# Kernel tuning notes

Hardware: AMD Instinct MI355X
Metric: run time of the kernel (lower is better)

Reference implementation:

```python
import jax, jax.numpy as jnp
import numpy as np

SR = 16000
FLEN = 400        # round(winlen * samplerate)
STEP = 160        # round(winstep * samplerate)
NFFT = 512
NFILT = 26
NUMCEP = 13
PREEMPH = 0.97
CEPLIFTER = 22
LOWFREQ = 0.0
HIGHFREQ = SR / 2.0
EPS = float(np.finfo(np.float32).eps)


def _hz2mel(hz):
    return 2595.0 * np.log10(1.0 + hz / 700.0)


def _mel2hz(mel):
    return 700.0 * (10.0 ** (mel / 2595.0) - 1.0)


def _filterbanks():
    # [NFFT//2+1, NFILT] mel triangular filterbank (transposed, as used in torch.mm)
    melpoints = np.linspace(_hz2mel(LOWFREQ), _hz2mel(HIGHFREQ), NFILT + 2)
    bins = np.floor((NFFT + 1) * _mel2hz(melpoints) / SR)
    fb = np.zeros([NFILT, NFFT // 2 + 1], dtype=np.float64)
    for j in range(NFILT):
        for i in range(int(bins[j]), int(bins[j + 1])):
            fb[j, i] = (i - bins[j]) / (bins[j + 1] - bins[j])
        for i in range(int(bins[j + 1]), int(bins[j + 2])):
            fb[j, i] = (bins[j + 2] - i) / (bins[j + 2] - bins[j + 1])
    return fb.T  # [257, 26]


def _dct_mat(N, k):
    # orthonormal DCT-II matrix rows 0..k-1: [k, N]
    n = np.arange(N)
    kk = np.arange(k)[:, None]
    C = np.cos(np.pi * (2 * n[None, :] + 1) * kk / (2.0 * N))
    C[0] *= 1.0 / np.sqrt(N)
    C[1:] *= np.sqrt(2.0 / N)
    return C


def setup_inputs() -> dict:
    key = jax.random.key(0)
    k1, k2 = jax.random.split(key)
    signals = jax.random.normal(k1, (64, 320000), dtype=jnp.float32)
    lengths = jax.random.randint(k2, (64,), 0, 320000, dtype=jnp.int32)
    return {"signals": signals, "lengths": lengths}


def reference(signals, lengths):
    B, T = signals.shape
    F = 1 if T <= FLEN else 1 + int(np.ceil((T - FLEN) / float(STEP)))
    padlen = (F - 1) * STEP + FLEN

    # preemphasis (uses self.preemph=0.97), masked past each sample's length
    pre = jnp.concatenate(
        [signals[:, :1], signals[:, 1:] - PREEMPH * signals[:, :-1]], axis=1)
    pos = jnp.arange(T)
    pre = jnp.where(pos[None, :] < lengths[:, None], pre, jnp.zeros((), pre.dtype))

    # framing: [B, F, FLEN]
    pad = jnp.pad(pre, ((0, 0), (0, padlen - T)))
    idx = np.arange(FLEN)[None, :] + STEP * np.arange(F)[:, None]
    frames = pad[:, idx]

    # power spectrum, [B, F, NFFT//2+1]
    spec = jnp.fft.rfft(frames, n=NFFT, axis=-1)
    pspec = (spec.real * spec.real + spec.imag * spec.imag) / NFFT
    energy = pspec.sum(-1) + EPS                      # [B, F]

    fb = jnp.asarray(_filterbanks(), dtype=signals.dtype)     # [257, 26]
    feat = jnp.log(pspec @ fb + EPS)                  # [B, F, 26]

    dctm = jnp.asarray(_dct_mat(NFILT, NUMCEP), dtype=signals.dtype)  # [13, 26]
    ceps = jnp.einsum('bfn,kn->bfk', feat, dctm)      # [B, F, 13]

    n = jnp.arange(NUMCEP, dtype=signals.dtype)
    lift = 1.0 + (CEPLIFTER / 2.0) * jnp.sin(np.pi * n / CEPLIFTER)
    ceps = ceps * lift
    ceps = ceps.at[:, :, 0].set(jnp.log(energy))       # appendEnergy

    # per-sample number of frames; zero-pad rest (original pads to batch max)
    nframes = jnp.where(
        lengths <= FLEN, 1,
        1 + jnp.ceil((lengths - FLEN) / float(STEP)).astype(jnp.int32))
    fmask = jnp.arange(F)[None, :] < nframes[:, None]
    ceps = jnp.where(fmask[:, :, None], ceps, jnp.zeros((), ceps.dtype))
    return ceps, nframes
```

## Files before the change

kernel.cpp:

```cpp
#include <hip/hip_runtime.h>
#include <math.h>

#define SRATE   16000
#define FLEN    400
#define STEP    160
#define NFFT    512
#define NBINS   257
#define NFILT   26
#define NUMCEP  13
#define BATCH   64
#define TLEN    320000
#define NFRAMES 1999
#define NPAIRS  1000
#define EPSF    1.1920929e-07f
#define PI_F    3.14159265358979323846f

typedef float    v2f __attribute__((ext_vector_type(2)));
typedef unsigned uv2 __attribute__((ext_vector_type(2)));

__device__ __forceinline__ v2f mk2(float a, float b) { v2f v; v.x = a; v.y = b; return v; }
__device__ __forceinline__ v2f pfma(v2f a, v2f b, v2f c) { return __builtin_elementwise_fma(a, b, c); }

template<int CTRL>
__device__ __forceinline__ float fdpp(float x) {
    return __builtin_bit_cast(float, __builtin_amdgcn_mov_dpp(
        __builtin_bit_cast(int, x), CTRL, 0xF, 0xF, true));
}
template<int IMM>
__device__ __forceinline__ float fswz(float x) {
    return __builtin_bit_cast(float, __builtin_amdgcn_ds_swizzle(
        __builtin_bit_cast(int, x), IMM));
}
__device__ __forceinline__ uv2 pl32(float x) {
    unsigned u = __builtin_bit_cast(unsigned, x);
    return __builtin_amdgcn_permlane32_swap(u, u, false, false);
}
__device__ __forceinline__ float fxor32(float x, bool hi32) {
    uv2 r = pl32(x);
    return __builtin_bit_cast(float, hi32 ? r[0] : r[1]);
}
#define DPP_X1   0xB1
#define DPP_X2   0x4E
#define DPP_X8   0x128
#define SWZ_X4   0x101F
#define SWZ_X16  0x401F

__global__ void mfcc_setup_kernel(const int* __restrict__ lengths,
                                  void* __restrict__ ws,
                                  float* __restrict__ out_nframes) {
    int tid = threadIdx.x;
    int*   bins = (int*)ws;
    float* dctw = (float*)ws + 32;

    if (tid < 28) {
        double M    = 2595.0 * log10(1.0 + 8000.0 / 700.0);
        double step = M / 27.0;
        double mel  = (tid == 27) ? M : (double)tid * step;
        double hz   = 700.0 * (pow(10.0, mel / 2595.0) - 1.0);
        bins[tid] = (int)floor((double)(NFFT + 1) * hz / (double)SRATE);
    }
    for (int t = tid; t < NUMCEP * NFILT; t += 64) {
        int k = t / NFILT, j = t - k * NFILT;
        double v = cos(M_PI * (double)((2 * j + 1) * k) / (2.0 * (double)NFILT));
        v *= (k == 0) ? 1.0 / sqrt((double)NFILT) : sqrt(2.0 / (double)NFILT);
        double lift = 1.0 + 11.0 * sin(M_PI * (double)k / 22.0);
        dctw[t] = (float)(v * lift);
    }
    if (tid < BATCH) {
        int len = lengths[tid];
        int nf  = (len <= FLEN) ? 1 : 1 + (len - FLEN + STEP - 1) / STEP;
        out_nframes[tid] = (float)nf;
    }
}

__launch_bounds__(256)
__global__ void mfcc_kernel(const float* __restrict__ sig,
                            const int*   __restrict__ lengths,
                            const void*  __restrict__ ws,
                            float*       __restrict__ out) {
    __shared__ float ps0[4][NBINS + 3];
    __shared__ float ps1[4][NBINS + 3];
    __shared__ float feat0[4][28], feat1[4][28];
    __shared__ float dctS[NUMCEP * NFILT];
    __shared__ int   binsS[NFILT + 2];

    const int tid  = threadIdx.x;
    const int lane = tid & 63;
    const int w    = tid >> 6;

    {
        const int*   binsG = (const int*)ws;
        const float* dctG  = (const float*)ws + 32;
        for (int t = tid; t < NUMCEP * NFILT; t += 256) dctS[t] = dctG[t];
        if (tid < NFILT + 2) binsS[tid] = binsG[tid];
    }
    __syncthreads();

    const int gp = blockIdx.x * 4 + w;
    const int b  = gp / NPAIRS;
    const int g  = gp - b * NPAIRS;
    const int f0 = 2 * g;
    const int f1 = f0 + 1;
    const int len = lengths[b];
    const int nf  = (len <= FLEN) ? 1 : 1 + (len - FLEN + STEP - 1) / STEP;

    if (f0 >= nf) {
        int k = lane & 31;
        bool hi = lane >= 32;
        int f = hi ? f1 : f0;
        if (k < NUMCEP && f < NFRAMES)
            out[((long)b * NFRAMES + f) * NUMCEP + k] = 0.0f;
        return;
    }

    const float* s = sig + (long)b * TLEN;
    const int base = f0 * STEP;

    const int B   = (int)(__brev((unsigned)lane) >> 26);
    const int i0  = 8 * B;
    const bool liveB = (i0 < FLEN);

    v2f Zr[4], Zi[4];
    const bool fastw = (base >= 1) && (base + 560 <= len);
    if (fastw) {
        float w0[9], w1[9];
        if (liveB) {
            const int tb0 = base + i0 - 1;
            #pragma unroll
            for (int j = 0; j < 9; ++j) {
                w0[j] = s[tb0 + j];
                w1[j] = s[tb0 + STEP + j];
            }
        } else {
            #pragma unroll
            for (int j = 0; j < 9; ++j) { w0[j] = 0.0f; w1[j] = 0.0f; }
        }
        #pragma unroll
        for (int m = 0; m < 4; ++m) {
            const int j = (m == 0) ? 0 : (m == 1) ? 4 : (m == 2) ? 2 : 6;
            Zr[m] = mk2(fmaf(-0.97f, w0[j],     w0[j + 1]),
                        fmaf(-0.97f, w0[j + 1], w0[j + 2]));
            Zi[m] = mk2(fmaf(-0.97f, w1[j],     w1[j + 1]),
                        fmaf(-0.97f, w1[j + 1], w1[j + 2]));
        }
    } else {
        float w0[9], w1[9];
        const int tb0 = base + i0 - 1;
        const int tb1 = tb0 + STEP;
        #pragma unroll
        for (int j = 0; j < 9; ++j) {
            int t0 = tb0 + j;
            w0[j] = (liveB && t0 >= 0 && t0 < len) ? s[t0] : 0.0f;
            int t1 = tb1 + j;
            w1[j] = (liveB && t1 < len) ? s[t1] : 0.0f;
        }
        const int tbe = base + i0;
        #pragma unroll
        for (int m = 0; m < 4; ++m) {
            const int j = (m == 0) ? 0 : (m == 1) ? 4 : (m == 2) ? 2 : 6;
            float v0a = fmaf(-0.97f, w0[j],     w0[j + 1]);
            float v0b = fmaf(-0.97f, w0[j + 1], w0[j + 2]);
            float v1a = fmaf(-0.97f, w1[j],     w1[j + 1]);
            float v1b = fmaf(-0.97f, w1[j + 1], w1[j + 2]);
            bool ma = liveB && (tbe + j) < len;
            bool mb = liveB && (tbe + j + 1) < len;
            bool na = liveB && (tbe + STEP + j) < len;
            bool nb = liveB && (tbe + STEP + j + 1) < len;
            Zr[m] = mk2(ma ? v0a : 0.0f, mb ? v0b : 0.0f);
            Zi[m] = mk2(na ? v1a : 0.0f, nb ? v1b : 0.0f);
        }
    }

    const float ang = -PI_F * (float)lane / 256.0f;
    float T1i = __sinf(ang);
    float T1r = __cosf(ang);
#define SQC(orr, oii, ir, ii) { float _r = ir * ir - ii * ii; oii = 2.0f * ir * ii; orr = _r; }
    float T2r, T2i;   SQC(T2r, T2i, T1r, T1i)
    float T4r, T4i;   SQC(T4r, T4i, T2r, T2i)
    float T8r, T8i;   SQC(T8r, T8i, T4r, T4i)
    float T16r, T16i; SQC(T16r, T16i, T8r, T8i)
    float T32r, T32i; SQC(T32r, T32i, T16r, T16i)
    float T64r, T64i; SQC(T64r, T64i, T32r, T32i)
    float T128r, T128i; SQC(T128r, T128i, T64r, T64i)
    const float RH = 0.70710678118654752f;
    const float A1r = RH * (T1r + T1i), A1i = RH * (T1i - T1r);
    const float A2r = T1i,              A2i = -T1r;
    const float A3r = RH * (T1i - T1r), A3i = -RH * (T1r + T1i);

    {
        const float sg = (lane & 1) ? -1.0f : 1.0f;
        const v2f sg2 = mk2(sg, sg);
        #pragma unroll
        for (int m = 0; m < 4; ++m) {
            v2f pr = mk2(fdpp<DPP_X1>(Zr[m].x), fdpp<DPP_X1>(Zr[m].y));
            v2f pi = mk2(fdpp<DPP_X1>(Zi[m].x), fdpp<DPP_X1>(Zi[m].y));
            Zr[m] = pfma(sg2, Zr[m], pr);
            Zi[m] = pfma(sg2, Zi[m], pi);
        }
    }

#define PK_XSTAGE_G(d, UR, UI, SH)                                            \
    {                                                                         \
        const bool hi_ = (lane & (d)) != 0;                                   \
        const float ur = hi_ ? (UR) : 1.0f;                                   \
        const float ui = hi_ ? (UI) : 0.0f;                                   \
        const float sg = hi_ ? 1.0f : -1.0f;                                  \
        const v2f ur2 = mk2(ur, ur), ui2 = mk2(ui, ui);                       \
        const v2f nui2 = mk2(-ui, -ui), sg2 = mk2(sg, sg);                    \
        _Pragma("unroll")                                                     \
        for (int m = 0; m < 4; ++m) {                                         \
            v2f tr = pfma(Zi[m], nui2, Zr[m] * ur2);                          \
            v2f ti = pfma(Zi[m], ur2,  Zr[m] * ui2);                          \
            v2f pr = mk2(SH(tr.x), SH(tr.y));                                 \
            v2f pi = mk2(SH(ti.x), SH(ti.y));                                 \
            Zr[m] = pfma(sg2, pr, tr);                                        \
            Zi[m] = pfma(sg2, pi, ti);                                        \
        }                                                                     \
    }
#define SH_X2(v)  fdpp<DPP_X2>(v)
#define SH_X4(v)  fswz<SWZ_X4>(v)
#define SH_X8(v)  fdpp<DPP_X8>(v)
#define SH_X16(v) fswz<SWZ_X16>(v)
#define SH_X32(v) fxor32(v, hi_)
    PK_XSTAGE_G(2,  T128r, T128i, SH_X2)
    PK_XSTAGE_G(4,  T64r,  T64i,  SH_X4)
    PK_XSTAGE_G(8,  T32r,  T32i,  SH_X8)
    PK_XSTAGE_G(16, T16r,  T16i,  SH_X16)
    PK_XSTAGE_G(32, T8r,   T8i,   SH_X32)

#define PBFLY(A, Bv, WR, WI)                                                  \
    {                                                                         \
        const v2f wr2 = mk2((WR), (WR)), wi2 = mk2((WI), (WI));               \
        const v2f nwi2 = mk2(-(WI), -(WI));                                   \
        v2f tr = pfma(Zi[Bv], nwi2, Zr[Bv] * wr2);                            \
        v2f ti = pfma(Zi[Bv], wr2,  Zr[Bv] * wi2);                            \
        Zr[Bv] = Zr[A] - tr;  Zi[Bv] = Zi[A] - ti;                            \
        Zr[A]  = Zr[A] + tr;  Zi[A]  = Zi[A] + ti;                            \
    }
    PBFLY(0, 1, T4r, T4i)
    PBFLY(2, 3, T4r, T4i)
    PBFLY(0, 2, T2r, T2i)
    PBFLY(1, 3, T2i, -T2r)

    float zr[8], zi[8];
    {
        #pragma unroll
        for (int m = 0; m < 4; ++m) {
            const float Wr = (m == 0) ? T1r : (m == 1) ? A1r : (m == 2) ? A2r : A3r;
            const float Wi = (m == 0) ? T1i : (m == 1) ? A1i : (m == 2) ? A2i : A3i;
            float tr = Zr[m].y * Wr - Zi[m].y * Wi;
            float ti = Zr[m].y * Wi + Zi[m].y * Wr;
            zr[m]     = Zr[m].x + tr;  zi[m]     = Zi[m].x + ti;
            zr[m + 4] = Zr[m].x - tr;  zi[m + 4] = Zi[m].x - ti;
        }
    }

    float* P0 = ps0[w];
    float* P1 = ps1[w];
    const float inv = 1.0f / (4.0f * (float)NFFT);
    float e0 = 0.0f, e1 = 0.0f;
    const int ml = (64 - lane) & 63;
    #pragma unroll
    for (int r = 0; r < 4; ++r) {
        float mr = __shfl(zr[7 - r], ml);
        float mi = __shfl(zi[7 - r], ml);
        if (lane == 0) { mr = zr[(8 - r) & 7]; mi = zi[(8 - r) & 7]; }
        float ar = zr[r] + mr, ai = zi[r] - mi;
        float br = zi[r] + mi, bi = zr[r] - mr;
        float p0 = (ar * ar + ai * ai) * inv;
        float p1 = (br * br + bi * bi) * inv;
        P0[64 * r + lane] = p0;
        P1[64 * r + lane] = p1;
        e0 += p0; e1 += p1;
    }
    if (lane == 0) {
        float p0 = 4.0f * zr[4] * zr[4] * inv;
        float p1 = 4.0f * zi[4] * zi[4] * inv;
        P0[256] = p0; P1[256] = p1;
        e0 += p0; e1 += p1;
    }
    v2f E = mk2(e0, e1);
    E = E + mk2(fdpp<DPP_X1>(E.x),  fdpp<DPP_X1>(E.y));
    E = E + mk2(fdpp<DPP_X2>(E.x),  fdpp<DPP_X2>(E.y));
    E = E + mk2(fswz<SWZ_X4>(E.x),  fswz<SWZ_X4>(E.y));
    E = E + mk2(fdpp<DPP_X8>(E.x),  fdpp<DPP_X8>(E.y));
    E = E + mk2(fswz<SWZ_X16>(E.x), fswz<SWZ_X16>(E.y));
    {
        uv2 rx = pl32(E.x), ry = pl32(E.y);
        E = mk2(__builtin_bit_cast(float, rx[0]) + __builtin_bit_cast(float, rx[1]),
                __builtin_bit_cast(float, ry[0]) + __builtin_bit_cast(float, ry[1]));
    }
    __builtin_amdgcn_wave_barrier();

    const int  j  = lane & 31;
    const bool hi = lane >= 32;
    {
        const float* P = hi ? P1 : P0;
        float fu = 0.0f, fs = 0.0f, fu2 = 0.0f, fs2 = 0.0f;
        if (j <= NFILT) {
            int bA = binsS[j], bB = binsS[j + 1];
            int i = bA;
            for (; i + 1 < bB; i += 2) {
                float p = P[i], q = P[i + 1];
                fs  += p;  fu  = fmaf(p, (float)(i - bA), fu);
                fs2 += q;  fu2 = fmaf(q, (float)(i + 1 - bA), fu2);
            }
            if (i < bB) {
                float p = P[i];
                fs += p;  fu = fmaf(p, (float)(i - bA), fu);
            }
            fs += fs2;  fu += fu2;
            fu *= (bB > bA) ? 1.0f / (float)(bB - bA) : 0.0f;
        }
        float down  = fs - fu;
        float dnext = __shfl(down, lane + 1);
        if (j < NFILT) {
            float fv = logf(fu + dnext + EPSF);
            if (hi) feat1[w][j] = fv; else feat0[w][j] = fv;
        }
    }
    __builtin_amdgcn_wave_barrier();

    if (j < NUMCEP) {
        const float* ft = hi ? feat1[w] : feat0[w];
        float a0 = 0.0f, a1 = 0.0f;
        #pragma unroll
        for (int jj = 0; jj < NFILT; jj += 2) {
            a0 = fmaf(ft[jj],     dctS[j * NFILT + jj],     a0);
            a1 = fmaf(ft[jj + 1], dctS[j * NFILT + jj + 1], a1);
        }
        float val = a0 + a1;
        if (j == 0) val = logf((hi ? E.y : E.x) + EPSF);
        int f = hi ? f1 : f0;
        if (f < NFRAMES) {
            if (f >= nf) val = 0.0f;
            out[((long)b * NFRAMES + f) * NUMCEP + j] = val;
        }
    }
}

extern "C" void kernel_launch(void* const* d_in, const int* in_sizes, int n_in,
                              void* d_out, int out_size, void* d_ws, size_t ws_size,
                              hipStream_t stream) {
    const float* sig     = (const float*)d_in[0];
    const int*   lengths = (const int*)d_in[1];
    float* out = (float*)d_out;

    mfcc_setup_kernel<<<1, 64, 0, stream>>>(lengths, d_ws,
                                            out + (size_t)BATCH * NFRAMES * NUMCEP);

    const int total_pairs = BATCH * NPAIRS;
    mfcc_kernel<<<total_pairs / 4, 256, 0, stream>>>(sig, lengths, d_ws, out);
}
```

Measured before the change: 56.69 us.

## Process four frames per wavefront with two interleaved packed FFTs

Each wavefront now handles four frames (two real-pair FFTs) instead of two. The FFT stages, power spectrum, filterbank and DCT are interleaved across both pairs with packed v2f math, and the grid shrinks by half. The intent is more independent work per wave to hide DPP/shuffle latency and to amortise twiddle setup, shared-table loads and per-wave overhead. The trade-off is higher register pressure, which may reduce occupancy. It also switches the log calls to fast __logf.

```diff
diff --git a/kernel.cpp b/kernel.cpp
--- a/kernel.cpp
+++ b/kernel.cpp
@@ -11,7 +11,7 @@
 #define BATCH   64
 #define TLEN    320000
 #define NFRAMES 1999
-#define NPAIRS  1000
+#define NGRP    500
 #define EPSF    1.1920929e-07f
 #define PI_F    3.14159265358979323846f
 
@@ -78,9 +78,9 @@
                             const int*   __restrict__ lengths,
                             const void*  __restrict__ ws,
                             float*       __restrict__ out) {
-    __shared__ float ps0[4][NBINS + 3];
-    __shared__ float ps1[4][NBINS + 3];
-    __shared__ float feat0[4][28], feat1[4][28];
+    __shared__ v2f psA[4][260];
+    __shared__ v2f psB[4][260];
+    __shared__ v2f featAs[4][28], featBs[4][28];
     __shared__ float dctS[NUMCEP * NFILT];
     __shared__ int   binsS[NFILT + 2];
 
@@ -96,20 +96,21 @@
     }
     __syncthreads();
 
-    const int gp = blockIdx.x * 4 + w;
-    const int b  = gp / NPAIRS;
-    const int g  = gp - b * NPAIRS;
-    const int f0 = 2 * g;
-    const int f1 = f0 + 1;
+    const int G  = blockIdx.x * 4 + w;
+    const int b  = G / NGRP;
+    const int q  = G - b * NGRP;
+    const int f0 = 4 * q;
     const int len = lengths[b];
     const int nf  = (len <= FLEN) ? 1 : 1 + (len - FLEN + STEP - 1) / STEP;
 
     if (f0 >= nf) {
-        int k = lane & 31;
-        bool hi = lane >= 32;
-        int f = hi ? f1 : f0;
-        if (k < NUMCEP && f < NFRAMES)
-            out[((long)b * NFRAMES + f) * NUMCEP + k] = 0.0f;
+        if (lane < 52) {
+            int d13 = lane / 13;
+            int kk  = lane - 13 * d13;
+            int ff  = f0 + d13;
+            if (ff < NFRAMES)
+                out[((long)b * NFRAMES + ff) * NUMCEP + kk] = 0.0f;
+        }
         return;
     }
 
@@ -120,54 +121,61 @@
     const int i0  = 8 * B;
     const bool liveB = (i0 < FLEN);
 
-    v2f Zr[4], Zi[4];
-    const bool fastw = (base >= 1) && (base + 560 <= len);
+    v2f Zr0[4], Zi0[4], Zr1[4], Zi1[4];
+    const bool fastw = (base >= 1) && (base + 880 <= len);
     if (fastw) {
-        float w0[9], w1[9];
+        float w0[9], w1[9], w2[9], w3[9];
         if (liveB) {
             const int tb0 = base + i0 - 1;
             #pragma unroll
             for (int j = 0; j < 9; ++j) {
                 w0[j] = s[tb0 + j];
-                w1[j] = s[tb0 + STEP + j];
+                w1[j] = s[tb0 + 160 + j];
+                w2[j] = s[tb0 + 320 + j];
+                w3[j] = s[tb0 + 480 + j];
             }
         } else {
             #pragma unroll
-            for (int j = 0; j < 9; ++j) { w0[j] = 0.0f; w1[j] = 0.0f; }
+            for (int j = 0; j < 9; ++j) { w0[j] = w1[j] = w2[j] = w3[j] = 0.0f; }
         }
         #pragma unroll
         for (int m = 0; m < 4; ++m) {
             const int j = (m == 0) ? 0 : (m == 1) ? 4 : (m == 2) ? 2 : 6;
-            Zr[m] = mk2(fmaf(-0.97f, w0[j],     w0[j + 1]),
-                        fmaf(-0.97f, w0[j + 1], w0[j + 2]));
-            Zi[m] = mk2(fmaf(-0.97f, w1[j],     w1[j + 1]),
-                        fmaf(-0.97f, w1[j + 1], w1[j + 2]));
+            Zr0[m] = mk2(fmaf(-0.97f, w0[j],     w0[j + 1]),
+                         fmaf(-0.97f, w0[j + 1], w0[j + 2]));
+            Zi0[m] = mk2(fmaf(-0.97f, w1[j],     w1[j + 1]),
+                         fmaf(-0.97f, w1[j + 1], w1[j + 2]));
+            Zr1[m] = mk2(fmaf(-0.97f, w2[j],     w2[j + 1]),
+                         fmaf(-0.97f, w2[j + 1], w2[j + 2]));
+            Zi1[m] = mk2(fmaf(-0.97f, w3[j],     w3[j + 1]),
+                         fmaf(-0.97f, w3[j + 1], w3[j + 2]));
         }
     } else {
-        float w0[9], w1[9];
+        float w0[9], w1[9], w2[9], w3[9];
         const int tb0 = base + i0 - 1;
-        const int tb1 = tb0 + STEP;
         #pragma unroll
         for (int j = 0; j < 9; ++j) {
             int t0 = tb0 + j;
             w0[j] = (liveB && t0 >= 0 && t0 < len) ? s[t0] : 0.0f;
-            int t1 = tb1 + j;
-            w1[j] = (liveB && t1 < len) ? s[t1] : 0.0f;
+            int t1 = t0 + 160; w1[j] = (liveB && t1 < len) ? s[t1] : 0.0f;
+            int t2 = t0 + 320; w2[j] = (liveB && t2 < len) ? s[t2] : 0.0f;
+            int t3 = t0 + 480; w3[j] = (liveB && t3 < len) ? s[t3] : 0.0f;
         }
         const int tbe = base + i0;
         #pragma unroll
         for (int m = 0; m < 4; ++m) {
             const int j = (m == 0) ? 0 : (m == 1) ? 4 : (m == 2) ? 2 : 6;
-            float v0a = fmaf(-0.97f, w0[j],     w0[j + 1]);
-            float v0b = fmaf(-0.97f, w0[j + 1], w0[j + 2]);
-            float v1a = fmaf(-0.97f, w1[j],     w1[j + 1]);
-            float v1b = fmaf(-0.97f, w1[j + 1], w1[j + 2]);
-            bool ma = liveB && (tbe + j) < len;
-            bool mb = liveB && (tbe + j + 1) < len;
-            bool na = liveB && (tbe + STEP + j) < len;
-            bool nb = liveB && (tbe + STEP + j + 1) < len;
-            Zr[m] = mk2(ma ? v0a : 0.0f, mb ? v0b : 0.0f);
-            Zi[m] = mk2(na ? v1a : 0.0f, nb ? v1b : 0.0f);
+#define ASMW(Wk, OFF, DST)                                                    \
+            { float va = fmaf(-0.97f, Wk[j],     Wk[j + 1]);                  \
+              float vb = fmaf(-0.97f, Wk[j + 1], Wk[j + 2]);                  \
+              bool ma = liveB && (tbe + (OFF) + j)     < len;                 \
+              bool mb = liveB && (tbe + (OFF) + j + 1) < len;                 \
+              DST = mk2(ma ? va : 0.0f, mb ? vb : 0.0f); }
+            ASMW(w0, 0,   Zr0[m])
+            ASMW(w1, 160, Zi0[m])
+            ASMW(w2, 320, Zr1[m])
+            ASMW(w3, 480, Zi1[m])
+#undef ASMW
         }
     }
 
@@ -192,14 +200,21 @@
         const v2f sg2 = mk2(sg, sg);
         #pragma unroll
         for (int m = 0; m < 4; ++m) {
-            v2f pr = mk2(fdpp<DPP_X1>(Zr[m].x), fdpp<DPP_X1>(Zr[m].y));
-            v2f pi = mk2(fdpp<DPP_X1>(Zi[m].x), fdpp<DPP_X1>(Zi[m].y));
-            Zr[m] = pfma(sg2, Zr[m], pr);
-            Zi[m] = pfma(sg2, Zi[m], pi);
-        }
-    }
-
-#define PK_XSTAGE_G(d, UR, UI, SH)                                            \
+            v2f pr = mk2(fdpp<DPP_X1>(Zr0[m].x), fdpp<DPP_X1>(Zr0[m].y));
+            v2f pi = mk2(fdpp<DPP_X1>(Zi0[m].x), fdpp<DPP_X1>(Zi0[m].y));
+            Zr0[m] = pfma(sg2, Zr0[m], pr);
+            Zi0[m] = pfma(sg2, Zi0[m], pi);
+        }
+        #pragma unroll
+        for (int m = 0; m < 4; ++m) {
+            v2f pr = mk2(fdpp<DPP_X1>(Zr1[m].x), fdpp<DPP_X1>(Zr1[m].y));
+            v2f pi = mk2(fdpp<DPP_X1>(Zi1[m].x), fdpp<DPP_X1>(Zi1[m].y));
+            Zr1[m] = pfma(sg2, Zr1[m], pr);
+            Zi1[m] = pfma(sg2, Zi1[m], pi);
+        }
+    }
+
+#define PK_XSTAGE2(d, UR, UI, SH)                                             \
     {                                                                         \
         const bool hi_ = (lane & (d)) != 0;                                   \
         const float ur = hi_ ? (UR) : 1.0f;                                   \
@@ -209,12 +224,21 @@
         const v2f nui2 = mk2(-ui, -ui), sg2 = mk2(sg, sg);                    \
         _Pragma("unroll")                                                     \
         for (int m = 0; m < 4; ++m) {                                         \
-            v2f tr = pfma(Zi[m], nui2, Zr[m] * ur2);                          \
-            v2f ti = pfma(Zi[m], ur2,  Zr[m] * ui2);                          \
+            v2f tr = pfma(Zi0[m], nui2, Zr0[m] * ur2);                        \
+            v2f ti = pfma(Zi0[m], ur2,  Zr0[m] * ui2);                        \
             v2f pr = mk2(SH(tr.x), SH(tr.y));                                 \
             v2f pi = mk2(SH(ti.x), SH(ti.y));                                 \
-            Zr[m] = pfma(sg2, pr, tr);                                        \
-            Zi[m] = pfma(sg2, pi, ti);                                        \
+            Zr0[m] = pfma(sg2, pr, tr);                                       \
+            Zi0[m] = pfma(sg2, pi, ti);                                       \
+        }                                                                     \
+        _Pragma("unroll")                                                     \
+        for (int m = 0; m < 4; ++m) {                                         \
+            v2f tr = pfma(Zi1[m], nui2, Zr1[m] * ur2);                        \
+            v2f ti = pfma(Zi1[m], ur2,  Zr1[m] * ui2);                        \
+            v2f pr = mk2(SH(tr.x), SH(tr.y));                                 \
+            v2f pi = mk2(SH(ti.x), SH(ti.y));                                 \
+            Zr1[m] = pfma(sg2, pr, tr);                                       \
+            Zi1[m] = pfma(sg2, pi, ti);                                       \
         }                                                                     \
     }
 #define SH_X2(v)  fdpp<DPP_X2>(v)
@@ -222,120 +246,137 @@
 #define SH_X8(v)  fdpp<DPP_X8>(v)
 #define SH_X16(v) fswz<SWZ_X16>(v)
 #define SH_X32(v) fxor32(v, hi_)
-    PK_XSTAGE_G(2,  T128r, T128i, SH_X2)
-    PK_XSTAGE_G(4,  T64r,  T64i,  SH_X4)
-    PK_XSTAGE_G(8,  T32r,  T32i,  SH_X8)
-    PK_XSTAGE_G(16, T16r,  T16i,  SH_X16)
-    PK_XSTAGE_G(32, T8r,   T8i,   SH_X32)
-
-#define PBFLY(A, Bv, WR, WI)                                                  \
+    PK_XSTAGE2(2,  T128r, T128i, SH_X2)
+    PK_XSTAGE2(4,  T64r,  T64i,  SH_X4)
+    PK_XSTAGE2(8,  T32r,  T32i,  SH_X8)
+    PK_XSTAGE2(16, T16r,  T16i,  SH_X16)
+    PK_XSTAGE2(32, T8r,   T8i,   SH_X32)
+
+#define PBFLY2(A, Bv, WR, WI)                                                 \
     {                                                                         \
         const v2f wr2 = mk2((WR), (WR)), wi2 = mk2((WI), (WI));               \
         const v2f nwi2 = mk2(-(WI), -(WI));                                   \
-        v2f tr = pfma(Zi[Bv], nwi2, Zr[Bv] * wr2);                            \
-        v2f ti = pfma(Zi[Bv], wr2,  Zr[Bv] * wi2);                            \
-        Zr[Bv] = Zr[A] - tr;  Zi[Bv] = Zi[A] - ti;                            \
-        Zr[A]  = Zr[A] + tr;  Zi[A]  = Zi[A] + ti;                            \
-    }
-    PBFLY(0, 1, T4r, T4i)
-    PBFLY(2, 3, T4r, T4i)
-    PBFLY(0, 2, T2r, T2i)
-    PBFLY(1, 3, T2i, -T2r)
-
-    float zr[8], zi[8];
-    {
-        #pragma unroll
-        for (int m = 0; m < 4; ++m) {
-            const float Wr = (m == 0) ? T1r : (m == 1) ? A1r : (m == 2) ? A2r : A3r;
-            const float Wi = (m == 0) ? T1i : (m == 1) ? A1i : (m == 2) ? A2i : A3i;
-            float tr = Zr[m].y * Wr - Zi[m].y * Wi;
-            float ti = Zr[m].y * Wi + Zi[m].y * Wr;
-            zr[m]     = Zr[m].x + tr;  zi[m]     = Zi[m].x + ti;
-            zr[m + 4] = Zr[m].x - tr;  zi[m + 4] = Zi[m].x - ti;
-        }
-    }
-
-    float* P0 = ps0[w];
-    float* P1 = ps1[w];
+        { v2f tr = pfma(Zi0[Bv], nwi2, Zr0[Bv] * wr2);                        \
+          v2f ti = pfma(Zi0[Bv], wr2,  Zr0[Bv] * wi2);                        \
+          Zr0[Bv] = Zr0[A] - tr;  Zi0[Bv] = Zi0[A] - ti;                      \
+          Zr0[A]  = Zr0[A] + tr;  Zi0[A]  = Zi0[A] + ti; }                    \
+        { v2f tr = pfma(Zi1[Bv], nwi2, Zr1[Bv] * wr2);                        \
+          v2f ti = pfma(Zi1[Bv], wr2,  Zr1[Bv] * wi2);                        \
+          Zr1[Bv] = Zr1[A] - tr;  Zi1[Bv] = Zi1[A] - ti;                      \
+          Zr1[A]  = Zr1[A] + tr;  Zi1[A]  = Zi1[A] + ti; }                    \
+    }
+    PBFLY2(0, 1, T4r, T4i)
+    PBFLY2(2, 3, T4r, T4i)
+    PBFLY2(0, 2, T2r, T2i)
+    PBFLY2(1, 3, T2i, -T2r)
+
+    float zrA[8], ziA[8], zrB[8], ziB[8];
+    #pragma unroll
+    for (int m = 0; m < 4; ++m) {
+        const float Wr = (m == 0) ? T1r : (m == 1) ? A1r : (m == 2) ? A2r : A3r;
+        const float Wi = (m == 0) ? T1i : (m == 1) ? A1i : (m == 2) ? A2i : A3i;
+        { float tr = Zr0[m].y * Wr - Zi0[m].y * Wi;
+          float ti = Zr0[m].y * Wi + Zi0[m].y * Wr;
+          zrA[m]     = Zr0[m].x + tr;  ziA[m]     = Zi0[m].x + ti;
+          zrA[m + 4] = Zr0[m].x - tr;  ziA[m + 4] = Zi0[m].x - ti; }
+        { float tr = Zr1[m].y * Wr - Zi1[m].y * Wi;
+          float ti = Zr1[m].y * Wi + Zi1[m].y * Wr;
+          zrB[m]     = Zr1[m].x + tr;  ziB[m]     = Zi1[m].x + ti;
+          zrB[m + 4] = Zr1[m].x - tr;  ziB[m + 4] = Zi1[m].x - ti; }
+    }
+
+    v2f* PA = psA[w];
+    v2f* PB = psB[w];
     const float inv = 1.0f / (4.0f * (float)NFFT);
-    float e0 = 0.0f, e1 = 0.0f;
+    v2f eA = mk2(0.0f, 0.0f), eB = mk2(0.0f, 0.0f);
     const int ml = (64 - lane) & 63;
     #pragma unroll
     for (int r = 0; r < 4; ++r) {
-        float mr = __shfl(zr[7 - r], ml);
-        float mi = __shfl(zi[7 - r], ml);
-        if (lane == 0) { mr = zr[(8 - r) & 7]; mi = zi[(8 - r) & 7]; }
-        float ar = zr[r] + mr, ai = zi[r] - mi;
-        float br = zi[r] + mi, bi = zr[r] - mr;
-        float p0 = (ar * ar + ai * ai) * inv;
-        float p1 = (br * br + bi * bi) * inv;
-        P0[64 * r + lane] = p0;
-        P1[64 * r + lane] = p1;
-        e0 += p0; e1 += p1;
+        float mrA = __shfl(zrA[7 - r], ml), miA = __shfl(ziA[7 - r], ml);
+        float mrB = __shfl(zrB[7 - r], ml), miB = __shfl(ziB[7 - r], ml);
+        if (lane == 0) {
+            mrA = zrA[(8 - r) & 7]; miA = ziA[(8 - r) & 7];
+            mrB = zrB[(8 - r) & 7]; miB = ziB[(8 - r) & 7];
+        }
+        { float ar = zrA[r] + mrA, ai = ziA[r] - miA;
+          float br = ziA[r] + miA, bi = zrA[r] - mrA;
+          v2f p = mk2((ar * ar + ai * ai) * inv, (br * br + bi * bi) * inv);
+          PA[64 * r + lane] = p;  eA += p; }
+        { float ar = zrB[r] + mrB, ai = ziB[r] - miB;
+          float br = ziB[r] + miB, bi = zrB[r] - mrB;
+          v2f p = mk2((ar * ar + ai * ai) * inv, (br * br + bi * bi) * inv);
+          PB[64 * r + lane] = p;  eB += p; }
     }
     if (lane == 0) {
-        float p0 = 4.0f * zr[4] * zr[4] * inv;
-        float p1 = 4.0f * zi[4] * zi[4] * inv;
-        P0[256] = p0; P1[256] = p1;
-        e0 += p0; e1 += p1;
-    }
-    v2f E = mk2(e0, e1);
-    E = E + mk2(fdpp<DPP_X1>(E.x),  fdpp<DPP_X1>(E.y));
-    E = E + mk2(fdpp<DPP_X2>(E.x),  fdpp<DPP_X2>(E.y));
-    E = E + mk2(fswz<SWZ_X4>(E.x),  fswz<SWZ_X4>(E.y));
-    E = E + mk2(fdpp<DPP_X8>(E.x),  fdpp<DPP_X8>(E.y));
-    E = E + mk2(fswz<SWZ_X16>(E.x), fswz<SWZ_X16>(E.y));
-    {
-        uv2 rx = pl32(E.x), ry = pl32(E.y);
-        E = mk2(__builtin_bit_cast(float, rx[0]) + __builtin_bit_cast(float, rx[1]),
-                __builtin_bit_cast(float, ry[0]) + __builtin_bit_cast(float, ry[1]));
-    }
+        v2f pA = mk2(4.0f * zrA[4] * zrA[4] * inv, 4.0f * ziA[4] * ziA[4] * inv);
+        v2f pB = mk2(4.0f * zrB[4] * zrB[4] * inv, 4.0f * ziB[4] * ziB[4] * inv);
+        PA[256] = pA;  eA += pA;
+        PB[256] = pB;  eB += pB;
+    }
+#define ERED(E)                                                               \
+    E = E + mk2(fdpp<DPP_X1>(E.x),  fdpp<DPP_X1>(E.y));                       \
+    E = E + mk2(fdpp<DPP_X2>(E.x),  fdpp<DPP_X2>(E.y));                       \
+    E = E + mk2(fswz<SWZ_X4>(E.x),  fswz<SWZ_X4>(E.y));                       \
+    E = E + mk2(fdpp<DPP_X8>(E.x),  fdpp<DPP_X8>(E.y));                       \
+    E = E + mk2(fswz<SWZ_X16>(E.x), fswz<SWZ_X16>(E.y));                      \
+    { uv2 rx = pl32(E.x), ry = pl32(E.y);                                     \
+      E = mk2(__builtin_bit_cast(float, rx[0]) + __builtin_bit_cast(float, rx[1]), \
+              __builtin_bit_cast(float, ry[0]) + __builtin_bit_cast(float, ry[1])); }
+    ERED(eA)
+    ERED(eB)
     __builtin_amdgcn_wave_barrier();
 
     const int  j  = lane & 31;
     const bool hi = lane >= 32;
     {
-        const float* P = hi ? P1 : P0;
-        float fu = 0.0f, fs = 0.0f, fu2 = 0.0f, fs2 = 0.0f;
+        const v2f* P = hi ? PB : PA;
+        v2f fu = mk2(0, 0), fs = mk2(0, 0), fu2 = mk2(0, 0), fs2 = mk2(0, 0);
         if (j <= NFILT) {
-            int bA = binsS[j], bB = binsS[j + 1];
+            int bA = binsS[j], bZ = binsS[j + 1];
             int i = bA;
-            for (; i + 1 < bB; i += 2) {
-                float p = P[i], q = P[i + 1];
-                fs  += p;  fu  = fmaf(p, (float)(i - bA), fu);
-                fs2 += q;  fu2 = fmaf(q, (float)(i + 1 - bA), fu2);
+            for (; i + 1 < bZ; i += 2) {
+                v2f p = P[i], p2 = P[i + 1];
+                float c0 = (float)(i - bA), c1 = (float)(i + 1 - bA);
+                fs  += p;   fu  = pfma(p,  mk2(c0, c0), fu);
+                fs2 += p2;  fu2 = pfma(p2, mk2(c1, c1), fu2);
             }
-            if (i < bB) {
-                float p = P[i];
-                fs += p;  fu = fmaf(p, (float)(i - bA), fu);
+            if (i < bZ) {
+                v2f p = P[i];
+                float c0 = (float)(i - bA);
+                fs += p;  fu = pfma(p, mk2(c0, c0), fu);
             }
             fs += fs2;  fu += fu2;
-            fu *= (bB > bA) ? 1.0f / (float)(bB - bA) : 0.0f;
-        }
-        float down  = fs - fu;
-        float dnext = __shfl(down, lane + 1);
+            float iw = (bZ > bA) ? 1.0f / (float)(bZ - bA) : 0.0f;
+            fu = fu * mk2(iw, iw);
+        }
+        v2f down = fs - fu;
+        v2f dn = mk2(__shfl(down.x, lane + 1), __shfl(down.y, lane + 1));
         if (j < NFILT) {
-            float fv = logf(fu + dnext + EPSF);
-            if (hi) feat1[w][j] = fv; else feat0[w][j] = fv;
+            v2f ft = fu + dn;
+            v2f fv = mk2(__logf(ft.x + EPSF), __logf(ft.y + EPSF));
+            if (hi) featBs[w][j] = fv; else featAs[w][j] = fv;
         }
     }
     __builtin_amdgcn_wave_barrier();
 
     if (j < NUMCEP) {
-        const float* ft = hi ? feat1[w] : feat0[w];
-        float a0 = 0.0f, a1 = 0.0f;
+        const v2f* ft = hi ? featBs[w] : featAs[w];
+        v2f a0 = mk2(0, 0), a1 = mk2(0, 0);
         #pragma unroll
         for (int jj = 0; jj < NFILT; jj += 2) {
-            a0 = fmaf(ft[jj],     dctS[j * NFILT + jj],     a0);
-            a1 = fmaf(ft[jj + 1], dctS[j * NFILT + jj + 1], a1);
-        }
-        float val = a0 + a1;
-        if (j == 0) val = logf((hi ? E.y : E.x) + EPSF);
-        int f = hi ? f1 : f0;
-        if (f < NFRAMES) {
-            if (f >= nf) val = 0.0f;
-            out[((long)b * NFRAMES + f) * NUMCEP + j] = val;
-        }
+            float c0 = dctS[j * NFILT + jj], c1 = dctS[j * NFILT + jj + 1];
+            a0 = pfma(ft[jj],     mk2(c0, c0), a0);
+            a1 = pfma(ft[jj + 1], mk2(c1, c1), a1);
+        }
+        v2f val = a0 + a1;
+        if (j == 0) {
+            v2f E = hi ? eB : eA;
+            val = mk2(__logf(E.x + EPSF), __logf(E.y + EPSF));
+        }
+        const int fb = f0 + (hi ? 2 : 0);
+        long o0 = ((long)b * NFRAMES + fb) * NUMCEP + j;
+        if (fb < NFRAMES)     out[o0]          = (fb     >= nf) ? 0.0f : val.x;
+        if (fb + 1 < NFRAMES) out[o0 + NUMCEP] = (fb + 1 >= nf) ? 0.0f : val.y;
     }
 }
 
@@ -349,6 +390,6 @@
     mfcc_setup_kernel<<<1, 64, 0, stream>>>(lengths, d_ws,
                                             out + (size_t)BATCH * NFRAMES * NUMCEP);
 
-    const int total_pairs = BATCH * NPAIRS;
-    mfcc_kernel<<<total_pairs / 4, 256, 0, stream>>>(sig, lengths, d_ws, out);
-}
+    const int total_groups = BATCH * NGRP;
+    mfcc_kernel<<<total_groups / 4, 256, 0, stream>>>(sig, lengths, d_ws, out);
+}
```

Result: faster. 51.61 us (-9.0%).
